# Kernel optimization log

Measured on AMD Instinct MI355X. Metric: run time of the kernel, lower is better.

The kernel has to match this reference:

```python
import jax, jax.numpy as jnp
import numpy as np

N_NODES = 50000
N_EDGES = 1_600_000
D_IN, D_HID, D_OUT, K = 128, 50, 10, 5


def setup_inputs() -> dict:
    key = jax.random.key(0)
    ks = jax.random.split(key, 6)
    x = jax.random.normal(ks[0], (N_NODES, D_IN), dtype=jnp.float32)
    edge_index = jax.random.randint(ks[1], (2, N_EDGES), 0, N_NODES, dtype=jnp.int64)
    cheb_w = jax.random.normal(ks[2], (K, D_IN, D_HID), dtype=jnp.float32) * 0.05
    cheb_b = jax.random.normal(ks[3], (D_HID,), dtype=jnp.float32) * 0.05
    fc_w = jax.random.normal(ks[4], (D_HID, D_OUT), dtype=jnp.float32) * 0.1
    fc_b = jax.random.normal(ks[5], (D_OUT,), dtype=jnp.float32) * 0.1
    return {"x": x, "edge_index": edge_index, "cheb_w": cheb_w,
            "cheb_b": cheb_b, "fc_w": fc_w, "fc_b": fc_b}


def reference(x, edge_index, cheb_w, cheb_b, fc_w, fc_b):
    # ChebConv (PyG, normalization='sym', lambda_max=2.0):
    # L_hat = 2L/lambda_max - I = -D^{-1/2} A D^{-1/2} (zero diagonal)
    row, col = edge_index[0], edge_index[1]
    n = x.shape[0]
    deg = jax.ops.segment_sum(jnp.ones_like(row, dtype=x.dtype), row, num_segments=n)
    dinv = jnp.where(deg > 0, jax.lax.rsqrt(jnp.maximum(deg, 1.0)), 0.0)
    w = -dinv[row] * dinv[col]  # [E] edge weights of L_hat

    def prop(h):  # L_hat @ h via gather-scale-scatter
        return jax.ops.segment_sum(w[:, None] * h[col], row, num_segments=n)

    tx0 = x
    tx1 = prop(x)
    out = jnp.einsum('ni,io->no', tx0, cheb_w[0]) + jnp.einsum('ni,io->no', tx1, cheb_w[1])
    for k in range(2, K):
        tx2 = 2.0 * prop(tx1) - tx0
        out = out + jnp.einsum('ni,io->no', tx2, cheb_w[k])
        tx0, tx1 = tx1, tx2
    out = out + cheb_b

    h = jax.nn.relu(out)
    logits = h @ fc_w + fc_b
    return jax.nn.log_softmax(logits, axis=1)
```

## Files before the change

kernel.cpp:

```cpp
#include <hip/hip_runtime.h>
#include <hip/hip_fp16.h>

#define N_NODES 50000
#define N_EDGES 1600000
#define D_IN    128
#define D_HID   50
#define D_OUT   10
#define K_CHEB  5

#define WH_ELEMS  (K_CHEB * 64 * D_IN)
#define WH_BLOCKS ((WH_ELEMS + 255) / 256)
#define XH_BLOCKS (N_NODES * D_IN / 8 / 256)

#define P1S_BLOCKS 1000
#define EPB        (N_EDGES / P1S_BLOCKS)
#define NBUCK      256
#define NB_USED    196
#define BCAP       32

#define VROW      64
#define VSTRIDE   ((size_t)(N_NODES + 1) * VROW)

#define NGROUP    (N_NODES / 16)
#define VG_SPAN   512
#define VG_WAVES  (K_CHEB * VG_SPAN)
#define VGB_BLOCKS (VG_WAVES / 16)

typedef _Float16 half8_t __attribute__((ext_vector_type(8)));
typedef float    f32x4_t __attribute__((ext_vector_type(4)));


__global__ __launch_bounds__(256) void buildA_kernel(const int* __restrict__ row,
                                                     const int* __restrict__ col,
                                                     unsigned int* __restrict__ store,
                                                     int* __restrict__ bcnt,
                                                     const float* __restrict__ x,
                                                     const float* __restrict__ W,
                                                     __half* __restrict__ xh,
                                                     __half* __restrict__ Wh,
                                                     __half* __restrict__ u,
                                                     __half* __restrict__ b1,
                                                     __half* __restrict__ b3,
                                                     __half* __restrict__ b2,
                                                     float* __restrict__ dinv) {
    __shared__ int cnt[NBUCK];
    int tid = threadIdx.x;
    int blk = blockIdx.x;
    if (blk < P1S_BLOCKS) {
        cnt[tid] = 0;
        __syncthreads();
        int base = blk * EPB;
        size_t sb = (size_t)blk * (NBUCK * BCAP);
        for (int i = tid; i < EPB; i += 256) {
            int r = row[base + i];
            int c = col[base + i];
            int b = r >> 8;
            int pos = atomicAdd(&cnt[b], 1);
            if (pos >= BCAP) pos = BCAP - 1;
            store[sb + b * BCAP + pos] = ((unsigned int)(r & 255) << 16) | (unsigned int)c;
        }
        __syncthreads();
        bcnt[blk * NBUCK + tid] = cnt[tid];
        return;
    }
    int pb = blk - P1S_BLOCKS;
    if (pb < XH_BLOCKS) {
        size_t base = ((size_t)pb * 256 + tid) * 8;
        float4 a = *(const float4*)(x + base);
        float4 b = *(const float4*)(x + base + 4);
        half8_t h;
        h[0] = (_Float16)a.x; h[1] = (_Float16)a.y;
        h[2] = (_Float16)a.z; h[3] = (_Float16)a.w;
        h[4] = (_Float16)b.x; h[5] = (_Float16)b.y;
        h[6] = (_Float16)b.z; h[7] = (_Float16)b.w;
        *(half8_t*)(xh + base) = h;
    } else if (pb < XH_BLOCKS + WH_BLOCKS) {
        int idx = (pb - XH_BLOCKS) * 256 + tid;
        if (idx < WH_ELEMS) {
            int i = idx & 127;
            int n = (idx >> 7) & 63;
            int t = idx >> 13;
            float vv = (n < D_HID) ? W[t * D_IN * D_HID + i * D_HID + n] : 0.f;
            Wh[idx] = __float2half(vv);
        }
    } else {
        if (tid < VROW) {
            __half z = __float2half(0.f);
            u[4 * VSTRIDE + (size_t)N_NODES * VROW + tid] = z;
            b1[(size_t)N_NODES * VROW + tid] = z;
            b3[(size_t)N_NODES * VROW + tid] = z;
            b2[(size_t)N_NODES * VROW + tid] = z;
        }
        if (tid == 64) dinv[N_NODES] = 0.f;
    }
}

__global__ __launch_bounds__(1024) void buildB_kernel(const unsigned int* __restrict__ store,
                                                      const int* __restrict__ bcnt,
                                                      int* __restrict__ row_start,
                                                      float* __restrict__ dinv,
                                                      float* __restrict__ dinv2,
                                                      float* __restrict__ sdeg,
                                                      int* __restrict__ ewc,
                                                      const __half* __restrict__ xh,
                                                      const __half* __restrict__ Wh,
                                                      __half* __restrict__ u) {
    __shared__ int hist[256];
    __shared__ int off[256];
    __shared__ int fill[256];
    __shared__ int sb_part[1024];
    __shared__ int pscan[256];
    __shared__ int s_bbase;
    int tid = threadIdx.x;
    int blk = blockIdx.x;
    if (blk >= NB_USED) {
        int lane = tid & 63;
        int wv = __builtin_amdgcn_readfirstlane(tid >> 6);
        int w = (blk - NB_USED) * 16 + wv;
        int t = w / VG_SPAN;
        int idx = w - t * VG_SPAN;
        int m = lane & 15;
        int quad = lane >> 4;

        const __half* Wt = Wh + t * (64 * D_IN);
        half8_t afr[4][4];
        #pragma unroll
        for (int ks = 0; ks < 4; ++ks) {
            int ko = ks * 32 + quad * 8;
            #pragma unroll
            for (int jt = 0; jt < 4; ++jt)
                afr[ks][jt] = *(const half8_t*)(Wt + (jt * 16 + m) * D_IN + ko);
        }

        __half* ut = u + t * VSTRIDE;

        half8_t pf[4];
        int g = idx;
        {
            const __half* xr = xh + (size_t)(g * 16 + m) * D_IN;
            #pragma unroll
            for (int ks = 0; ks < 4; ++ks)
                pf[ks] = *(const half8_t*)(xr + ks * 32 + quad * 8);
        }

        for (; g < NGROUP; g += VG_SPAN) {
            int node = g * 16 + m;
            half8_t bfr[4];
            #pragma unroll
            for (int ks = 0; ks < 4; ++ks) bfr[ks] = pf[ks];
            int gn = g + VG_SPAN;
            if (gn < NGROUP) {
                const __half* xr = xh + (size_t)(gn * 16 + m) * D_IN;
                #pragma unroll
                for (int ks = 0; ks < 4; ++ks)
                    pf[ks] = *(const half8_t*)(xr + ks * 32 + quad * 8);
            }
            f32x4_t acc[4];
            #pragma unroll
            for (int jt = 0; jt < 4; ++jt) acc[jt] = (f32x4_t)0.f;
            #pragma unroll
            for (int ks = 0; ks < 4; ++ks)
                #pragma unroll
                for (int jt = 0; jt < 4; ++jt)
                    acc[jt] = __builtin_amdgcn_mfma_f32_16x16x32_f16(afr[ks][jt], bfr[ks], acc[jt], 0, 0, 0);
            __half* dst = ut + (size_t)node * VROW + quad * 4;
            #pragma unroll
            for (int jt = 0; jt < 4; ++jt) {
                __half2 h0 = __float22half2_rn(make_float2(acc[jt][0], acc[jt][1]));
                __half2 h1 = __float22half2_rn(make_float2(acc[jt][2], acc[jt][3]));
                uint2 uu;
                uu.x = *(unsigned int*)&h0;
                uu.y = *(unsigned int*)&h1;
                *(uint2*)(dst + jt * 16) = uu;
            }
        }
        return;
    }
    int b = blk;
    {
        int bt = tid & 255, seg = tid >> 8;
        int sum = 0;
        for (int s = seg * 250; s < seg * 250 + 250; ++s) sum += bcnt[s * NBUCK + bt];
        sb_part[tid] = sum;
    }
    __syncthreads();
    if (tid < 256) pscan[tid] = sb_part[tid] + sb_part[256 + tid]
                              + sb_part[512 + tid] + sb_part[768 + tid];
    __syncthreads();
    for (int o = 1; o < 256; o <<= 1) {
        int vv = (tid < 256 && tid >= o) ? pscan[tid - o] : 0;
        __syncthreads();
        if (tid < 256) pscan[tid] += vv;
        __syncthreads();
    }
    if (tid == 0) {
        s_bbase = (b == 0) ? 0 : pscan[b - 1];
        if (b == 0) row_start[N_NODES] = pscan[255];
    }
    if (tid < 256) hist[tid] = 0;
    __syncthreads();
    int bbase_b = s_bbase;

    int sn = 0;
    size_t sb = 0;
    if (tid < P1S_BLOCKS) {
        sn = bcnt[tid * NBUCK + b];
        sb = (size_t)tid * (NBUCK * BCAP) + b * BCAP;
    }
    for (int i = 0; i < sn; ++i)
        atomicAdd(&hist[store[sb + i] >> 16], 1);
    __syncthreads();
    int d = (tid < 256) ? hist[tid] : 0;
    if (tid < 256) off[tid] = d;
    __syncthreads();
    for (int o = 1; o < 256; o <<= 1) {
        int vv = (tid < 256 && tid >= o) ? off[tid - o] : 0;
        __syncthreads();
        if (tid < 256) off[tid] += vv;
        __syncthreads();
    }
    if (tid < 256) {
        int excl = off[tid] - d + bbase_b;
        hist[tid] = excl;
        fill[tid] = 0;
        int r = (b << 8) + tid;
        if (r < N_NODES) {
            row_start[r] = excl;
            float fd = (float)d;
            dinv[r]  = d ? rsqrtf(fd)  : 0.f;
            dinv2[r] = d ? (1.f / fd)  : 0.f;
            sdeg[r]  = d ? sqrtf(fd)   : 0.f;
        }
    }
    __syncthreads();
    for (int i = 0; i < sn; ++i) {
        unsigned int vv = store[sb + i];
        int rl = vv >> 16;
        int c = vv & 0xffff;
        int p = atomicAdd(&fill[rl], 1);
        ewc[hist[rl] + p] = c;
    }
}

template<int SCALE_SRC, int DO_SUB, int SCALE_SUB>
__global__ __launch_bounds__(512) void prop_kernel(const int* __restrict__ row_start,
                                                   const int* __restrict__ ewc,
                                                   const float* __restrict__ dinv2,
                                                   const float* __restrict__ dinv,
                                                   const __half* __restrict__ src,
                                                   const __half* __restrict__ addv,
                                                   const __half* __restrict__ subv,
                                                   float alphaM,
                                                   __half* __restrict__ dst) {
    int tid = threadIdx.x;
    int lane = tid & 63;
    int wv = __builtin_amdgcn_readfirstlane(tid >> 6);
    int r = blockIdx.x * 8 + wv;
    int e0 = row_start[r], e1 = row_start[r + 1];
    float fac = -alphaM * dinv2[r];
    int l = lane & 7;
    int g = lane >> 3;
    const uint4* src16 = (const uint4*)src;
    float ac[8];
    #pragma unroll
    for (int j = 0; j < 8; ++j) ac[j] = 0.f;
    for (int e = e0; e < e1; e += 16) {
        #pragma unroll
        for (int i = 0; i < 2; ++i) {
            int base = e + 8 * i;
            int cl = ewc[base + g];
            if (base + g >= e1) cl = N_NODES;
            uint4 uu = src16[(size_t)cl * 8 + l];
            float2 f0 = __half22float2(*(__half2*)&uu.x);
            float2 f1 = __half22float2(*(__half2*)&uu.y);
            float2 f2 = __half22float2(*(__half2*)&uu.z);
            float2 f3 = __half22float2(*(__half2*)&uu.w);
            if (SCALE_SRC) {
                float dc = dinv[cl];
                ac[0] = fmaf(dc, f0.x, ac[0]); ac[1] = fmaf(dc, f0.y, ac[1]);
                ac[2] = fmaf(dc, f1.x, ac[2]); ac[3] = fmaf(dc, f1.y, ac[3]);
                ac[4] = fmaf(dc, f2.x, ac[4]); ac[5] = fmaf(dc, f2.y, ac[5]);
                ac[6] = fmaf(dc, f3.x, ac[6]); ac[7] = fmaf(dc, f3.y, ac[7]);
            } else {
                ac[0] += f0.x; ac[1] += f0.y; ac[2] += f1.x; ac[3] += f1.y;
                ac[4] += f2.x; ac[5] += f2.y; ac[6] += f3.x; ac[7] += f3.y;
            }
        }
    }
    #pragma unroll
    for (int k = 8; k <= 32; k <<= 1) {
        #pragma unroll
        for (int j = 0; j < 8; ++j) ac[j] += __shfl_xor(ac[j], k);
    }
    if (g == 0) {
        float sa = dinv[r];
        size_t o = (size_t)r * 8 + l;
        uint4 av = ((const uint4*)addv)[o];
        float2 av0 = __half22float2(*(__half2*)&av.x);
        float2 av1 = __half22float2(*(__half2*)&av.y);
        float2 av2 = __half22float2(*(__half2*)&av.z);
        float2 av3 = __half22float2(*(__half2*)&av.w);
        float r0 = fmaf(sa, av0.x, fac * ac[0]);
        float r1 = fmaf(sa, av0.y, fac * ac[1]);
        float r2 = fmaf(sa, av1.x, fac * ac[2]);
        float r3 = fmaf(sa, av1.y, fac * ac[3]);
        float r4 = fmaf(sa, av2.x, fac * ac[4]);
        float r5 = fmaf(sa, av2.y, fac * ac[5]);
        float r6 = fmaf(sa, av3.x, fac * ac[6]);
        float r7 = fmaf(sa, av3.y, fac * ac[7]);
        if (DO_SUB) {
            float ss = SCALE_SUB ? dinv[r] : 1.f;
            uint4 sv = ((const uint4*)subv)[o];
            float2 sv0 = __half22float2(*(__half2*)&sv.x);
            float2 sv1 = __half22float2(*(__half2*)&sv.y);
            float2 sv2 = __half22float2(*(__half2*)&sv.z);
            float2 sv3 = __half22float2(*(__half2*)&sv.w);
            r0 = fmaf(-ss, sv0.x, r0); r1 = fmaf(-ss, sv0.y, r1);
            r2 = fmaf(-ss, sv1.x, r2); r3 = fmaf(-ss, sv1.y, r3);
            r4 = fmaf(-ss, sv2.x, r4); r5 = fmaf(-ss, sv2.y, r5);
            r6 = fmaf(-ss, sv3.x, r6); r7 = fmaf(-ss, sv3.y, r7);
        }
        __half2 h0 = __float22half2_rn(make_float2(r0, r1));
        __half2 h1 = __float22half2_rn(make_float2(r2, r3));
        __half2 h2 = __float22half2_rn(make_float2(r4, r5));
        __half2 h3 = __float22half2_rn(make_float2(r6, r7));
        uint4 uu;
        uu.x = *(unsigned int*)&h0;
        uu.y = *(unsigned int*)&h1;
        uu.z = *(unsigned int*)&h2;
        uu.w = *(unsigned int*)&h3;
        ((uint4*)dst)[o] = uu;
    }
}

__global__ __launch_bounds__(256) void final_kernel(const __half* __restrict__ S,
                                                    const float* __restrict__ sdeg,
                                                    const float* __restrict__ cheb_b,
                                                    const float* __restrict__ fc_w,
                                                    const float* __restrict__ fc_b,
                                                    float* __restrict__ out) {
    int r = blockIdx.x * blockDim.x + threadIdx.x;
    if (r >= N_NODES) return;
    float sc = sdeg[r];
    const __half2* s2 = (const __half2*)(S + (size_t)r * VROW);
    float h[D_HID];
    #pragma unroll
    for (int i = 0; i < D_HID / 2; ++i) {
        float2 f = __half22float2(s2[i]);
        float v0 = sc * f.x + cheb_b[2 * i];
        float v1 = sc * f.y + cheb_b[2 * i + 1];
        h[2 * i]     = v0 > 0.f ? v0 : 0.f;
        h[2 * i + 1] = v1 > 0.f ? v1 : 0.f;
    }
    float lg[D_OUT];
    #pragma unroll
    for (int o = 0; o < D_OUT; ++o) lg[o] = fc_b[o];
    #pragma unroll 2
    for (int i = 0; i < D_HID; ++i) {
        float hv = h[i];
        #pragma unroll
        for (int o = 0; o < D_OUT; ++o) lg[o] += hv * fc_w[i * D_OUT + o];
    }
    float mx = lg[0];
    #pragma unroll
    for (int o = 1; o < D_OUT; ++o) mx = fmaxf(mx, lg[o]);
    float s = 0.f;
    #pragma unroll
    for (int o = 0; o < D_OUT; ++o) s += __expf(lg[o] - mx);
    float ls = __logf(s);
    size_t oo = (size_t)r * D_OUT;
    #pragma unroll
    for (int o = 0; o < D_OUT; ++o) out[oo + o] = lg[o] - mx - ls;
}

extern "C" void kernel_launch(void* const* d_in, const int* in_sizes, int n_in,
                              void* d_out, int out_size, void* d_ws, size_t ws_size,
                              hipStream_t stream) {
    const float* x      = (const float*)d_in[0];
    const int*   edge   = (const int*)d_in[1];
    const float* cheb_w = (const float*)d_in[2];
    const float* cheb_b = (const float*)d_in[3];
    const float* fc_w   = (const float*)d_in[4];
    const float* fc_b   = (const float*)d_in[5];
    float* out = (float*)d_out;

    const int* erow = edge;
    const int* ecol = edge + N_EDGES;

    uintptr_t p = ((uintptr_t)d_ws + 255) & ~(uintptr_t)255;
    auto alloc = [&](size_t bytes) {
        uintptr_t q = p;
        p = (p + bytes + 255) & ~(uintptr_t)255;
        return (void*)q;
    };
    int*    row_start = (int*)alloc((size_t)(N_NODES + 1) * 4);
    float*  dinv      = (float*)alloc((size_t)(N_NODES + 1) * 4);
    float*  dinv2     = (float*)alloc((size_t)N_NODES * 4);
    float*  sdeg      = (float*)alloc((size_t)N_NODES * 4);
    int*    ewc       = (int*)alloc((size_t)(N_EDGES + 32) * 4);
    unsigned int* store = (unsigned int*)alloc((size_t)P1S_BLOCKS * NBUCK * BCAP * 4);
    int*    bcnt      = (int*)alloc((size_t)P1S_BLOCKS * NBUCK * 4);
    __half* Wh        = (__half*)alloc((size_t)WH_ELEMS * 2);
    __half* xh        = (__half*)alloc((size_t)N_NODES * D_IN * 2);
    __half* Sbuf      = (__half*)alloc(VSTRIDE * 2);
    __half* u         = (__half*)alloc(5 * VSTRIDE * 2);
    __half* b1        = (__half*)alloc(VSTRIDE * 2);
    __half* b3        = (__half*)alloc(VSTRIDE * 2);
    __half* b2        = (__half*)alloc(VSTRIDE * 2);
    __half* S  = Sbuf;

    buildA_kernel<<<P1S_BLOCKS + XH_BLOCKS + WH_BLOCKS + 1, 256, 0, stream>>>(
        erow, ecol, store, bcnt, x, cheb_w, xh, Wh, u, b1, b3, b2, dinv);

    buildB_kernel<<<NB_USED + VGB_BLOCKS, 1024, 0, stream>>>(
        store, bcnt, row_start, dinv, dinv2, sdeg, ewc, xh, Wh, u);

    __half* u0 = u;
    __half* u1 = u + 1 * VSTRIDE;
    __half* u2 = u + 2 * VSTRIDE;
    __half* u3 = u + 3 * VSTRIDE;
    __half* u4 = u + 4 * VSTRIDE;
    const int PB = N_NODES / 8;
    prop_kernel<1, 0, 0><<<PB, 512, 0, stream>>>(row_start, ewc, dinv2, dinv,
                                                 u4, u3, u3, 2.f, b3);
    prop_kernel<0, 1, 1><<<PB, 512, 0, stream>>>(row_start, ewc, dinv2, dinv,
                                                 b3, u2, u4, 2.f, b2);
    prop_kernel<0, 1, 0><<<PB, 512, 0, stream>>>(row_start, ewc, dinv2, dinv,
                                                 b2, u1, b3, 2.f, b1);
    prop_kernel<0, 1, 0><<<PB, 512, 0, stream>>>(row_start, ewc, dinv2, dinv,
                                                 b1, u0, b2, 1.f, S);

    final_kernel<<<(N_NODES + 255) / 256, 256, 0, stream>>>(S, sdeg, cheb_b,
                                                            fc_w, fc_b, out);
}
```

Baseline: 290.7 us.

## Hoist bucket prefix scan into a separate kernel, transpose bcnt, widen gather unroll

Before this change, each of the 196 bucket blocks in buildB redundantly summed all 256x1000 bucket counts and scanned them. That work now runs once in a small single-block scanB kernel, and bcnt is transposed so reads are contiguous per bucket. The prop gather loop now handles 32 edges per iteration instead of 16, and VG_SPAN doubles, which changes how many waves the MFMA projection in buildB uses. The cost is one extra kernel launch and serialization on the single-block scan.

```diff
diff --git a/kernel.cpp b/kernel.cpp
--- a/kernel.cpp
+++ b/kernel.cpp
@@ -22,7 +22,7 @@
 #define VSTRIDE   ((size_t)(N_NODES + 1) * VROW)
 
 #define NGROUP    (N_NODES / 16)
-#define VG_SPAN   512
+#define VG_SPAN   1024
 #define VG_WAVES  (K_CHEB * VG_SPAN)
 #define VGB_BLOCKS (VG_WAVES / 16)
 
@@ -60,7 +60,7 @@
             store[sb + b * BCAP + pos] = ((unsigned int)(r & 255) << 16) | (unsigned int)c;
         }
         __syncthreads();
-        bcnt[blk * NBUCK + tid] = cnt[tid];
+        bcnt[tid * P1S_BLOCKS + blk] = cnt[tid];
         return;
     }
     int pb = blk - P1S_BLOCKS;
@@ -95,8 +95,40 @@
     }
 }
 
+__global__ __launch_bounds__(1024) void scanB_kernel(const int* __restrict__ bcnt,
+                                                     int* __restrict__ bbase,
+                                                     int* __restrict__ row_start) {
+    __shared__ int part[1024];
+    __shared__ int tot[256];
+    int tid = threadIdx.x;
+    int b = tid >> 2, q = tid & 3;
+    const int* p = bcnt + b * P1S_BLOCKS + q * 250;
+    int s = 0;
+    #pragma unroll 5
+    for (int i = 0; i < 250; ++i) s += p[i];
+    part[tid] = s;
+    __syncthreads();
+    int db = 0;
+    if (tid < 256) {
+        db = part[4 * tid] + part[4 * tid + 1] + part[4 * tid + 2] + part[4 * tid + 3];
+        tot[tid] = db;
+    }
+    __syncthreads();
+    for (int o = 1; o < 256; o <<= 1) {
+        int v = (tid < 256 && tid >= o) ? tot[tid - o] : 0;
+        __syncthreads();
+        if (tid < 256) tot[tid] += v;
+        __syncthreads();
+    }
+    if (tid < 256) {
+        bbase[tid] = tot[tid] - db;
+        if (tid == 255) row_start[N_NODES] = tot[255];
+    }
+}
+
 __global__ __launch_bounds__(1024) void buildB_kernel(const unsigned int* __restrict__ store,
                                                       const int* __restrict__ bcnt,
+                                                      const int* __restrict__ bbase,
                                                       int* __restrict__ row_start,
                                                       float* __restrict__ dinv,
                                                       float* __restrict__ dinv2,
@@ -108,9 +140,6 @@
     __shared__ int hist[256];
     __shared__ int off[256];
     __shared__ int fill[256];
-    __shared__ int sb_part[1024];
-    __shared__ int pscan[256];
-    __shared__ int s_bbase;
     int tid = threadIdx.x;
     int blk = blockIdx.x;
     if (blk >= NB_USED) {
@@ -177,34 +206,14 @@
         return;
     }
     int b = blk;
-    {
-        int bt = tid & 255, seg = tid >> 8;
-        int sum = 0;
-        for (int s = seg * 250; s < seg * 250 + 250; ++s) sum += bcnt[s * NBUCK + bt];
-        sb_part[tid] = sum;
-    }
-    __syncthreads();
-    if (tid < 256) pscan[tid] = sb_part[tid] + sb_part[256 + tid]
-                              + sb_part[512 + tid] + sb_part[768 + tid];
-    __syncthreads();
-    for (int o = 1; o < 256; o <<= 1) {
-        int vv = (tid < 256 && tid >= o) ? pscan[tid - o] : 0;
-        __syncthreads();
-        if (tid < 256) pscan[tid] += vv;
-        __syncthreads();
-    }
-    if (tid == 0) {
-        s_bbase = (b == 0) ? 0 : pscan[b - 1];
-        if (b == 0) row_start[N_NODES] = pscan[255];
-    }
+    int bbase_b = bbase[b];
     if (tid < 256) hist[tid] = 0;
     __syncthreads();
-    int bbase_b = s_bbase;
 
     int sn = 0;
     size_t sb = 0;
     if (tid < P1S_BLOCKS) {
-        sn = bcnt[tid * NBUCK + b];
+        sn = bcnt[b * P1S_BLOCKS + tid];
         sb = (size_t)tid * (NBUCK * BCAP) + b * BCAP;
     }
     for (int i = 0; i < sn; ++i)
@@ -264,9 +273,9 @@
     float ac[8];
     #pragma unroll
     for (int j = 0; j < 8; ++j) ac[j] = 0.f;
-    for (int e = e0; e < e1; e += 16) {
+    for (int e = e0; e < e1; e += 32) {
         #pragma unroll
-        for (int i = 0; i < 2; ++i) {
+        for (int i = 0; i < 4; ++i) {
             int base = e + 8 * i;
             int cl = ewc[base + g];
             if (base + g >= e1) cl = N_NODES;
@@ -399,7 +408,8 @@
     float*  sdeg      = (float*)alloc((size_t)N_NODES * 4);
     int*    ewc       = (int*)alloc((size_t)(N_EDGES + 32) * 4);
     unsigned int* store = (unsigned int*)alloc((size_t)P1S_BLOCKS * NBUCK * BCAP * 4);
-    int*    bcnt      = (int*)alloc((size_t)P1S_BLOCKS * NBUCK * 4);
+    int*    bcnt      = (int*)alloc((size_t)NBUCK * P1S_BLOCKS * 4);
+    int*    bbase     = (int*)alloc((size_t)NBUCK * 4);
     __half* Wh        = (__half*)alloc((size_t)WH_ELEMS * 2);
     __half* xh        = (__half*)alloc((size_t)N_NODES * D_IN * 2);
     __half* Sbuf      = (__half*)alloc(VSTRIDE * 2);
@@ -412,8 +422,10 @@
     buildA_kernel<<<P1S_BLOCKS + XH_BLOCKS + WH_BLOCKS + 1, 256, 0, stream>>>(
         erow, ecol, store, bcnt, x, cheb_w, xh, Wh, u, b1, b3, b2, dinv);
 
+    scanB_kernel<<<1, 1024, 0, stream>>>(bcnt, bbase, row_start);
+
     buildB_kernel<<<NB_USED + VGB_BLOCKS, 1024, 0, stream>>>(
-        store, bcnt, row_start, dinv, dinv2, sdeg, ewc, xh, Wh, u);
+        store, bcnt, bbase, row_start, dinv, dinv2, sdeg, ewc, xh, Wh, u);
 
     __half* u0 = u;
     __half* u1 = u + 1 * VSTRIDE;
```

New measurement: 327.8 us. +12.8%, slower.
